# Performance work log

Measured on AMD Instinct MI355X. Metric: run time of the kernel, lower is better.

Reference implementation:

```python
import jax, jax.numpy as jnp
import numpy as np


def setup_inputs() -> dict:
    key = jax.random.key(0)
    k1, k2, k3 = jax.random.split(key, 3)
    B, S, D = 32, 1024, 256
    input_real = jax.random.normal(k1, (B, S, D), dtype=jnp.float32)
    input_imag = jax.random.normal(k2, (B, S, D), dtype=jnp.float32)
    # per-token mixture weights (e.g. softmax over sequence in CFN)
    weights = jax.random.uniform(k3, (B, S), dtype=jnp.float32)
    return {"input_real": input_real, "input_imag": input_imag, "weights": weights}


def reference(input_real, input_imag, weights):
    # Original layer: out[b,a,c] = sum_s w[b,s] * (v[b,s,a] * conj(v)[b,s,c]) with v = r + i*j
    # output_real[a,c] = r[a]r[c] + i[a]i[c];  output_imag[a,c] = i[a]r[c] - r[a]i[c]
    # Weighted sum over s == V^T diag(w) V, expressed as einsum (no (B,S,D,D) intermediate).
    wr = input_real * weights[:, :, None]  # (B,S,D)
    wi = input_imag * weights[:, :, None]
    output_r = jnp.einsum('bsa,bsc->bac', wr, input_real) + jnp.einsum('bsa,bsc->bac', wi, input_imag)
    output_i = jnp.einsum('bsa,bsc->bac', wi, input_real) - jnp.einsum('bsa,bsc->bac', wr, input_imag)
    return (output_r, output_i)
```

## Files before the change

kernel.cpp:

```cpp
#include <hip/hip_runtime.h>

typedef __attribute__((ext_vector_type(8))) short s8v;
typedef __attribute__((ext_vector_type(16))) float f32x16;

#define BB 32
#define SS 1024
#define DD 256
#define KB 32
#define NCH (SS / KB)
#define LSTR 40
#define PSZ (64 * LSTR)
#define BUFS (6 * PSZ)


__device__ __forceinline__ unsigned short bf16rn(float v) {
    unsigned b = __float_as_uint(v);
    return (unsigned short)((b + 0x7FFFu + ((b >> 16) & 1u)) >> 16);
}

extern "C" __global__ void __launch_bounds__(256, 2)
cmix4_kernel(const float* __restrict__ real, const float* __restrict__ imag,
             const float* __restrict__ wts, float* __restrict__ out) {
    __shared__ unsigned short lds[2 * BUFS];

    const int bx   = blockIdx.x;
    const int xcd  = bx & 7;
    const int slot = bx >> 3;
    const int b    = xcd * 4 + (slot >> 4);
    const int t    = slot & 15;
    const int a0   = (t >> 2) * 64;
    const int c0   = (t & 3) * 64;

    const int tid = threadIdx.x;
    const int wid = tid >> 6;
    const int l   = tid & 63;

    const int  fgrp = l >> 2;
    const int  sgrp = l & 3;
    const bool isA  = (wid < 2);
    const float* srcA = ((wid & 1) ? imag : real)
                      + (size_t)b * SS * DD + (isA ? a0 : c0) + fgrp * 4;
    const float* wb = wts + (size_t)b * SS;
    const int pA   = wid * 2 * PSZ;
    const int pC   = (4 + (wid & 1)) * PSZ;
    const int woff = fgrp * 4 * LSTR + sgrp * 8;

    const int m0  = (wid >> 1) * 32;
    const int n0  = (wid & 1) * 32;
    const int fr  = l & 31;
    const int hi8 = (l >> 5) * 8;

    f32x16 accr = {}, acci = {}, accx = {};
    float4 xr[8];

    auto stage_load = [&](int sch) {
        const int sh = sch + sgrp * 8;
        #pragma unroll
        for (int si = 0; si < 8; ++si)
            xr[si] = *(const float4*)(srcA + (size_t)(sh + si) * DD);
    };

    auto stage_store = [&](unsigned short* buf, int sch) {
        const int sh = sch + sgrp * 8;
        if (isA) {
            const float4 w1 = *(const float4*)(wb + sh);
            const float4 w2 = *(const float4*)(wb + sh + 4);
            const float wv[8] = {w1.x,w1.y,w1.z,w1.w,w2.x,w2.y,w2.z,w2.w};
            unsigned hw[4][4], lw[4][4];
            #pragma unroll
            for (int si = 0; si < 8; ++si) {
                const float y[4] = {xr[si].x*wv[si], xr[si].y*wv[si],
                                    xr[si].z*wv[si], xr[si].w*wv[si]};
                #pragma unroll
                for (int e = 0; e < 4; ++e) {
                    unsigned yb   = __float_as_uint(y[e]);
                    unsigned hb32 = yb & 0xFFFF0000u;
                    float    lo   = y[e] - __uint_as_float(hb32);
                    unsigned hs   = hb32 >> 16;
                    unsigned ls   = __float_as_uint(lo) >> 16;
                    if (si & 1) { hw[e][si>>1] |= hs << 16; lw[e][si>>1] |= ls << 16; }
                    else        { hw[e][si>>1]  = hs;       lw[e][si>>1]  = ls; }
                }
            }
            #pragma unroll
            for (int e = 0; e < 4; ++e) {
                uint4 vh = {hw[e][0], hw[e][1], hw[e][2], hw[e][3]};
                uint4 vl = {lw[e][0], lw[e][1], lw[e][2], lw[e][3]};
                *(uint4*)&buf[pA + woff + e * LSTR]       = vh;
                *(uint4*)&buf[pA + PSZ + woff + e * LSTR] = vl;
            }
        } else {
            unsigned cw[4][4];
            #pragma unroll
            for (int si = 0; si < 8; ++si) {
                const float y[4] = {xr[si].x, xr[si].y, xr[si].z, xr[si].w};
                #pragma unroll
                for (int e = 0; e < 4; ++e) {
                    unsigned cs = bf16rn(y[e]);
                    if (si & 1) cw[e][si>>1] |= cs << 16; else cw[e][si>>1] = cs;
                }
            }
            #pragma unroll
            for (int e = 0; e < 4; ++e) {
                uint4 v = {cw[e][0], cw[e][1], cw[e][2], cw[e][3]};
                *(uint4*)&buf[pC + woff + e * LSTR] = v;
            }
        }
    };

    stage_load(0);
    stage_store(lds, 0);
    __syncthreads();

    for (int ch = 0; ch < NCH; ++ch) {
        unsigned short* bc = lds + (ch & 1) * BUFS;
        unsigned short* bs = lds + ((ch & 1) ^ 1) * BUFS;
        const bool more = (ch + 1 < NCH);
        if (more) stage_load((ch + 1) * KB);

        #pragma unroll
        for (int kk = 0; kk < 2; ++kk) {
            const int ko = kk * 16 + hi8;
            const int ra = (m0 + fr) * LSTR + ko;
            const int rc = (n0 + fr) * LSTR + ko;
            s8v A1 = *(const s8v*)&bc[0*PSZ + ra];
            s8v A2 = *(const s8v*)&bc[1*PSZ + ra];
            s8v A3 = *(const s8v*)&bc[2*PSZ + ra];
            s8v A4 = *(const s8v*)&bc[3*PSZ + ra];
            s8v C1 = *(const s8v*)&bc[4*PSZ + rc];
            s8v C2 = *(const s8v*)&bc[5*PSZ + rc];
            accr = __builtin_amdgcn_mfma_f32_32x32x16_bf16(A1, C1, accr, 0, 0, 0);
            accr = __builtin_amdgcn_mfma_f32_32x32x16_bf16(A2, C1, accr, 0, 0, 0);
            accr = __builtin_amdgcn_mfma_f32_32x32x16_bf16(A3, C2, accr, 0, 0, 0);
            accr = __builtin_amdgcn_mfma_f32_32x32x16_bf16(A4, C2, accr, 0, 0, 0);
            acci = __builtin_amdgcn_mfma_f32_32x32x16_bf16(A3, C1, acci, 0, 0, 0);
            acci = __builtin_amdgcn_mfma_f32_32x32x16_bf16(A4, C1, acci, 0, 0, 0);
            accx = __builtin_amdgcn_mfma_f32_32x32x16_bf16(A1, C2, accx, 0, 0, 0);
            accx = __builtin_amdgcn_mfma_f32_32x32x16_bf16(A2, C2, accx, 0, 0, 0);
        }

        if (more) stage_store(bs, (ch + 1) * KB);
        __syncthreads();
    }

    float* outR = out + (size_t)b * DD * DD;
    float* outI = out + (size_t)BB * DD * DD + (size_t)b * DD * DD;
    const int col = c0 + n0 + (l & 31);
    #pragma unroll
    for (int g = 0; g < 4; ++g) {
        #pragma unroll
        for (int q = 0; q < 4; ++q) {
            const int reg = g * 4 + q;
            const int row = a0 + m0 + q + 8 * g + 4 * (l >> 5);
            outR[(size_t)row * DD + col] = accr[reg];
            outI[(size_t)row * DD + col] = acci[reg] - accx[reg];
        }
    }
}

extern "C" void kernel_launch(void* const* d_in, const int* in_sizes, int n_in,
                              void* d_out, int out_size, void* d_ws, size_t ws_size,
                              hipStream_t stream) {
    const float* real = (const float*)d_in[0];
    const float* imag = (const float*)d_in[1];
    const float* wts  = (const float*)d_in[2];
    float* out = (float*)d_out;
    dim3 grid(512);
    dim3 block(256);
    cmix4_kernel<<<grid, block, 0, stream>>>(real, imag, wts, out);
}
```

Measured before the change: 155.8 us.

## Split sequence reduction across two wave groups per block with LDS combine

Doubles the block to 512 threads and splits the 1024-long sequence into two halves, each reduced by its own group of four waves with a private LDS buffer. The K chunk shrinks to 16 with a narrower LDS stride, and the double buffer is replaced by a store, sync, compute, sync loop. The second group's partial accumulators go through LDS and are added by the first group before the global write. This aims to raise parallelism and hide load latency with more waves per CU, at the cost of two barriers per chunk and an extra reduction step.

Measured after the change: 171.4 us. +10.0%, slower.

```diff
diff --git a/kernel.cpp b/kernel.cpp
--- a/kernel.cpp
+++ b/kernel.cpp
@@ -6,11 +6,13 @@
 #define BB 32
 #define SS 1024
 #define DD 256
-#define KB 32
-#define NCH (SS / KB)
-#define LSTR 40
+#define KB 16
+#define KHALF 512
+#define NCH (KHALF / KB)
+#define LSTR 24
 #define PSZ (64 * LSTR)
-#define BUFS (6 * PSZ)
+#define BUFSZ (6 * PSZ)
+#define TOTSH (2 * BUFSZ)
 
 
 __device__ __forceinline__ unsigned short bf16rn(float v) {
@@ -18,10 +20,10 @@
     return (unsigned short)((b + 0x7FFFu + ((b >> 16) & 1u)) >> 16);
 }
 
-extern "C" __global__ void __launch_bounds__(256, 2)
-cmix4_kernel(const float* __restrict__ real, const float* __restrict__ imag,
+extern "C" __global__ void __launch_bounds__(512, 4)
+cmix6_kernel(const float* __restrict__ real, const float* __restrict__ imag,
              const float* __restrict__ wts, float* __restrict__ out) {
-    __shared__ unsigned short lds[2 * BUFS];
+    __shared__ unsigned short lds[TOTSH];
 
     const int bx   = blockIdx.x;
     const int xcd  = bx & 7;
@@ -33,127 +35,130 @@
 
     const int tid = threadIdx.x;
     const int wid = tid >> 6;
+    const int kg  = wid >> 2;
+    const int wq  = wid & 3;
     const int l   = tid & 63;
 
     const int  fgrp = l >> 2;
     const int  sgrp = l & 3;
-    const bool isA  = (wid < 2);
-    const float* srcA = ((wid & 1) ? imag : real)
+    const bool isA  = (wq < 2);
+    const float* srcA = ((wq & 1) ? imag : real)
                       + (size_t)b * SS * DD + (isA ? a0 : c0) + fgrp * 4;
     const float* wb = wts + (size_t)b * SS;
-    const int pA   = wid * 2 * PSZ;
-    const int pC   = (4 + (wid & 1)) * PSZ;
-    const int woff = fgrp * 4 * LSTR + sgrp * 8;
+    const int pA = wq * 2 * PSZ;
+    const int pC = (4 + (wq & 1)) * PSZ;
 
-    const int m0  = (wid >> 1) * 32;
-    const int n0  = (wid & 1) * 32;
+    const int m0  = (wq >> 1) * 32;
+    const int n0  = (wq & 1) * 32;
     const int fr  = l & 31;
     const int hi8 = (l >> 5) * 8;
 
+    unsigned short* klds = lds + kg * BUFSZ;
+    const int sbeg = kg * KHALF;
+
     f32x16 accr = {}, acci = {}, accx = {};
-    float4 xr[8];
+    float4 xr[4];
 
-    auto stage_load = [&](int sch) {
-        const int sh = sch + sgrp * 8;
+    auto stage_load = [&](int ch) {
+        const int sh = sbeg + ch * KB + sgrp * 4;
         #pragma unroll
-        for (int si = 0; si < 8; ++si)
+        for (int si = 0; si < 4; ++si)
             xr[si] = *(const float4*)(srcA + (size_t)(sh + si) * DD);
     };
 
-    auto stage_store = [&](unsigned short* buf, int sch) {
-        const int sh = sch + sgrp * 8;
+    auto stage_store = [&](int ch) {
+        const int sh = sbeg + ch * KB + sgrp * 4;
+        const float xs[4][4] = {
+            {xr[0].x, xr[0].y, xr[0].z, xr[0].w},
+            {xr[1].x, xr[1].y, xr[1].z, xr[1].w},
+            {xr[2].x, xr[2].y, xr[2].z, xr[2].w},
+            {xr[3].x, xr[3].y, xr[3].z, xr[3].w}};
         if (isA) {
-            const float4 w1 = *(const float4*)(wb + sh);
-            const float4 w2 = *(const float4*)(wb + sh + 4);
-            const float wv[8] = {w1.x,w1.y,w1.z,w1.w,w2.x,w2.y,w2.z,w2.w};
-            unsigned hw[4][4], lw[4][4];
-            #pragma unroll
-            for (int si = 0; si < 8; ++si) {
-                const float y[4] = {xr[si].x*wv[si], xr[si].y*wv[si],
-                                    xr[si].z*wv[si], xr[si].w*wv[si]};
-                #pragma unroll
-                for (int e = 0; e < 4; ++e) {
-                    unsigned yb   = __float_as_uint(y[e]);
-                    unsigned hb32 = yb & 0xFFFF0000u;
-                    float    lo   = y[e] - __uint_as_float(hb32);
-                    unsigned hs   = hb32 >> 16;
-                    unsigned ls   = __float_as_uint(lo) >> 16;
-                    if (si & 1) { hw[e][si>>1] |= hs << 16; lw[e][si>>1] |= ls << 16; }
-                    else        { hw[e][si>>1]  = hs;       lw[e][si>>1]  = ls; }
-                }
-            }
+            const float4 w4 = *(const float4*)(wb + sh);
+            const float wv[4] = {w4.x, w4.y, w4.z, w4.w};
             #pragma unroll
             for (int e = 0; e < 4; ++e) {
-                uint4 vh = {hw[e][0], hw[e][1], hw[e][2], hw[e][3]};
-                uint4 vl = {lw[e][0], lw[e][1], lw[e][2], lw[e][3]};
-                *(uint4*)&buf[pA + woff + e * LSTR]       = vh;
-                *(uint4*)&buf[pA + PSZ + woff + e * LSTR] = vl;
+                unsigned hs[4], ls[4];
+                #pragma unroll
+                for (int si = 0; si < 4; ++si) {
+                    const float y     = xs[si][e] * wv[si];
+                    const unsigned yb = __float_as_uint(y);
+                    const unsigned hb = yb & 0xFFFF0000u;
+                    const float    lo = y - __uint_as_float(hb);
+                    hs[si] = hb >> 16;
+                    ls[si] = __float_as_uint(lo) >> 16;
+                }
+                const int off = pA + (fgrp * 4 + e) * LSTR + sgrp * 4;
+                uint2 vh = {hs[0] | (hs[1] << 16), hs[2] | (hs[3] << 16)};
+                uint2 vl = {ls[0] | (ls[1] << 16), ls[2] | (ls[3] << 16)};
+                *(uint2*)&klds[off]       = vh;
+                *(uint2*)&klds[off + PSZ] = vl;
             }
         } else {
-            unsigned cw[4][4];
-            #pragma unroll
-            for (int si = 0; si < 8; ++si) {
-                const float y[4] = {xr[si].x, xr[si].y, xr[si].z, xr[si].w};
-                #pragma unroll
-                for (int e = 0; e < 4; ++e) {
-                    unsigned cs = bf16rn(y[e]);
-                    if (si & 1) cw[e][si>>1] |= cs << 16; else cw[e][si>>1] = cs;
-                }
-            }
             #pragma unroll
             for (int e = 0; e < 4; ++e) {
-                uint4 v = {cw[e][0], cw[e][1], cw[e][2], cw[e][3]};
-                *(uint4*)&buf[pC + woff + e * LSTR] = v;
+                unsigned cs[4];
+                #pragma unroll
+                for (int si = 0; si < 4; ++si) cs[si] = bf16rn(xs[si][e]);
+                const int off = pC + (fgrp * 4 + e) * LSTR + sgrp * 4;
+                uint2 v = {cs[0] | (cs[1] << 16), cs[2] | (cs[3] << 16)};
+                *(uint2*)&klds[off] = v;
             }
         }
     };
 
     stage_load(0);
-    stage_store(lds, 0);
-    __syncthreads();
 
     for (int ch = 0; ch < NCH; ++ch) {
-        unsigned short* bc = lds + (ch & 1) * BUFS;
-        unsigned short* bs = lds + ((ch & 1) ^ 1) * BUFS;
-        const bool more = (ch + 1 < NCH);
-        if (more) stage_load((ch + 1) * KB);
+        stage_store(ch);
+        __syncthreads();
+        if (ch + 1 < NCH) stage_load(ch + 1);
 
-        #pragma unroll
-        for (int kk = 0; kk < 2; ++kk) {
-            const int ko = kk * 16 + hi8;
-            const int ra = (m0 + fr) * LSTR + ko;
-            const int rc = (n0 + fr) * LSTR + ko;
-            s8v A1 = *(const s8v*)&bc[0*PSZ + ra];
-            s8v A2 = *(const s8v*)&bc[1*PSZ + ra];
-            s8v A3 = *(const s8v*)&bc[2*PSZ + ra];
-            s8v A4 = *(const s8v*)&bc[3*PSZ + ra];
-            s8v C1 = *(const s8v*)&bc[4*PSZ + rc];
-            s8v C2 = *(const s8v*)&bc[5*PSZ + rc];
-            accr = __builtin_amdgcn_mfma_f32_32x32x16_bf16(A1, C1, accr, 0, 0, 0);
-            accr = __builtin_amdgcn_mfma_f32_32x32x16_bf16(A2, C1, accr, 0, 0, 0);
-            accr = __builtin_amdgcn_mfma_f32_32x32x16_bf16(A3, C2, accr, 0, 0, 0);
-            accr = __builtin_amdgcn_mfma_f32_32x32x16_bf16(A4, C2, accr, 0, 0, 0);
-            acci = __builtin_amdgcn_mfma_f32_32x32x16_bf16(A3, C1, acci, 0, 0, 0);
-            acci = __builtin_amdgcn_mfma_f32_32x32x16_bf16(A4, C1, acci, 0, 0, 0);
-            accx = __builtin_amdgcn_mfma_f32_32x32x16_bf16(A1, C2, accx, 0, 0, 0);
-            accx = __builtin_amdgcn_mfma_f32_32x32x16_bf16(A2, C2, accx, 0, 0, 0);
-        }
+        const int ra = (m0 + fr) * LSTR + hi8;
+        const int rc = (n0 + fr) * LSTR + hi8;
+        s8v A1 = *(const s8v*)&klds[0 * PSZ + ra];
+        s8v A2 = *(const s8v*)&klds[1 * PSZ + ra];
+        s8v A3 = *(const s8v*)&klds[2 * PSZ + ra];
+        s8v A4 = *(const s8v*)&klds[3 * PSZ + ra];
+        s8v C1 = *(const s8v*)&klds[4 * PSZ + rc];
+        s8v C2 = *(const s8v*)&klds[5 * PSZ + rc];
+        accr = __builtin_amdgcn_mfma_f32_32x32x16_bf16(A1, C1, accr, 0, 0, 0);
+        accr = __builtin_amdgcn_mfma_f32_32x32x16_bf16(A2, C1, accr, 0, 0, 0);
+        accr = __builtin_amdgcn_mfma_f32_32x32x16_bf16(A3, C2, accr, 0, 0, 0);
+        accr = __builtin_amdgcn_mfma_f32_32x32x16_bf16(A4, C2, accr, 0, 0, 0);
+        acci = __builtin_amdgcn_mfma_f32_32x32x16_bf16(A3, C1, acci, 0, 0, 0);
+        acci = __builtin_amdgcn_mfma_f32_32x32x16_bf16(A4, C1, acci, 0, 0, 0);
+        accx = __builtin_amdgcn_mfma_f32_32x32x16_bf16(A1, C2, accx, 0, 0, 0);
+        accx = __builtin_amdgcn_mfma_f32_32x32x16_bf16(A2, C2, accx, 0, 0, 0);
 
-        if (more) stage_store(bs, (ch + 1) * KB);
         __syncthreads();
     }
 
-    float* outR = out + (size_t)b * DD * DD;
-    float* outI = out + (size_t)BB * DD * DD + (size_t)b * DD * DD;
-    const int col = c0 + n0 + (l & 31);
-    #pragma unroll
-    for (int g = 0; g < 4; ++g) {
+    float* ex = (float*)lds;
+    const int gl = wq * 64 + l;
+    if (kg == 1) {
         #pragma unroll
-        for (int q = 0; q < 4; ++q) {
-            const int reg = g * 4 + q;
-            const int row = a0 + m0 + q + 8 * g + 4 * (l >> 5);
-            outR[(size_t)row * DD + col] = accr[reg];
-            outI[(size_t)row * DD + col] = acci[reg] - accx[reg];
+        for (int j = 0; j < 16; ++j) {
+            ex[j * 256 + gl]        = accr[j];
+            ex[(16 + j) * 256 + gl] = acci[j] - accx[j];
+        }
+    }
+    __syncthreads();
+    if (kg == 0) {
+        float* outR = out + (size_t)b * DD * DD;
+        float* outI = out + (size_t)BB * DD * DD + (size_t)b * DD * DD;
+        const int col = c0 + n0 + (l & 31);
+        #pragma unroll
+        for (int g = 0; g < 4; ++g) {
+            #pragma unroll
+            for (int q = 0; q < 4; ++q) {
+                const int reg = g * 4 + q;
+                const int row = a0 + m0 + q + 8 * g + 4 * (l >> 5);
+                const float orr = accr[reg] + ex[reg * 256 + gl];
+                const float oii = (acci[reg] - accx[reg]) + ex[(16 + reg) * 256 + gl];
+                outR[(size_t)row * DD + col] = orr;
+                outI[(size_t)row * DD + col] = oii;
+            }
         }
     }
 }
@@ -166,6 +171,6 @@
     const float* wts  = (const float*)d_in[2];
     float* out = (float*)d_out;
     dim3 grid(512);
-    dim3 block(256);
-    cmix4_kernel<<<grid, block, 0, stream>>>(real, imag, wts, out);
+    dim3 block(512);
+    cmix6_kernel<<<grid, block, 0, stream>>>(real, imag, wts, out);
 }
```
